# Kernel tuning notes

Hardware: AMD Instinct MI355X
Metric: run time of the kernel (lower is better)

Reference implementation:

```python
import jax, jax.numpy as jnp
import numpy as np

D_MODEL = 1024
N_HEADS = 16
D_HEAD = D_MODEL // N_HEADS
MODES = 32


def setup_inputs() -> dict:
    key = jax.random.key(0)
    ks = jax.random.split(key, 7)
    B, L = 4, 4096
    s = 1.0 / np.sqrt(D_MODEL)
    return {
        "q_in": jax.random.normal(ks[0], (B, L, D_MODEL), dtype=jnp.float32),
        "Wv": jax.random.uniform(ks[1], (D_MODEL, D_MODEL), jnp.float32, -s, s),
        "bv": jax.random.uniform(ks[2], (D_MODEL,), jnp.float32, -s, s),
        "Wo": jax.random.uniform(ks[3], (D_MODEL, D_MODEL), jnp.float32, -s, s),
        "bo": jax.random.uniform(ks[4], (D_MODEL,), jnp.float32, -s, s),
        "w_real": jax.random.normal(ks[5], (N_HEADS, MODES, D_HEAD), dtype=jnp.float32) * 0.02,
        "w_imag": jax.random.normal(ks[6], (N_HEADS, MODES, D_HEAD), dtype=jnp.float32) * 0.02,
    }


def reference(q_in, Wv, bv, Wo, bo, w_real, w_imag):
    B, L, dm = q_in.shape
    # v projection -> [B, H, L, Dh]
    v = (q_in @ Wv.T + bv).reshape(B, L, N_HEADS, D_HEAD).transpose(0, 2, 1, 3)
    # rFFT over time axis; keep only lowest MODES frequencies
    v_ft = jnp.fft.rfft(v, axis=2)                      # [B, H, L//2+1, Dh] complex
    w = (w_real + 1j * w_imag)[None]                    # [1, H, MODES, Dh]
    out_ft = v_ft[:, :, :MODES, :] * w                  # truncated spectrum
    # irfft zero-pads the truncated spectrum up to n//2+1 (== torch's zeros_like + slice-assign)
    out = jnp.fft.irfft(out_ft, n=L, axis=2)            # [B, H, L, Dh]
    out = out.transpose(0, 2, 1, 3).reshape(B, L, dm)
    return out @ Wo.T + bo
```

## Files before the change

### kernel.cpp

```cpp
#include <hip/hip_runtime.h>
#include <math.h>


typedef __attribute__((ext_vector_type(8))) short bf16x8;
typedef __attribute__((ext_vector_type(8))) unsigned short ushort8;
typedef __attribute__((ext_vector_type(4))) float f32x4;

__device__ __forceinline__ unsigned short f2bf(float x) {
    union { float f; unsigned int u; } c; c.f = x;
    unsigned int u = c.u + 0x7FFFu + ((c.u >> 16) & 1u);
    return (unsigned short)(u >> 16);
}

__global__ __launch_bounds__(256) void k_init(unsigned short* __restrict__ F,
                                              unsigned short* __restrict__ G) {
    int idx = blockIdx.x * 256 + threadIdx.x;
    const float w0 = 1.5339807878856412e-3f;
    {
        int j = idx >> 12, t = idx & 4095, k = j >> 1;
        int r = (k * t) & 4095;
        float s, c; sincosf((float)r * w0, &s, &c);
        F[idx] = f2bf((j & 1) ? -s : c);
    }
    {
        int j = idx & 63, k = j >> 1;
        int t = idx >> 6;
        int r = (k * t) & 4095;
        float s, c; sincosf((float)r * w0, &s, &c);
        float ck = (k == 0) ? (1.0f / 4096.0f) : (2.0f / 4096.0f);
        float v = (j & 1) ? ((k == 0) ? 0.0f : -ck * s) : ck * c;
        G[idx] = f2bf(v);
    }
}

__global__ __launch_bounds__(64) void k_dft_fwd(const float* __restrict__ q,
                                                const unsigned short* __restrict__ F,
                                                float* __restrict__ P0) {
    __shared__ __align__(16) unsigned short Ft[64 * 40];
    __shared__ __align__(16) unsigned short qT[32 * 40];
    int blk = blockIdx.x;
    int kp = blk & 15, nt = (blk >> 4) & 31, b = blk >> 9;
    int n0 = nt * 32, t0 = kp * 256;
    int lane = threadIdx.x;
    int lm = lane & 15, q4 = lane >> 4;
    int nn4 = (lane & 7) * 4, th = lane >> 3;
    f32x4 acc[4][2] = {};
    for (int ks = 0; ks < 8; ++ks) {
        int tb = t0 + ks * 32;
        #pragma unroll
        for (int i = 0; i < 4; ++i) {
            ushort8 v = *(const ushort8*)&F[lane * 4096 + tb + i * 8];
            *(ushort8*)&Ft[lane * 40 + i * 8] = v;
        }
        #pragma unroll
        for (int r2 = 0; r2 < 2; ++r2) {
            int p = r2 * 8 + th;
            const float* row0 = &q[(size_t)(b * 4096 + tb + 2 * p) * 1024 + n0 + nn4];
            float4 v0 = *(const float4*)row0;
            float4 v1 = *(const float4*)(row0 + 1024);
            #pragma unroll
            for (int i = 0; i < 4; ++i) {
                float a = (&v0.x)[i], c = (&v1.x)[i];
                unsigned int u = (unsigned int)f2bf(a) | ((unsigned int)f2bf(c) << 16);
                *(unsigned int*)&qT[(nn4 + i) * 40 + 2 * p] = u;
            }
        }
        __syncthreads();
        bf16x8 af[4], bq[2];
        #pragma unroll
        for (int mt = 0; mt < 4; ++mt)
            af[mt] = *(const bf16x8*)&Ft[(mt * 16 + lm) * 40 + q4 * 8];
        #pragma unroll
        for (int ntt = 0; ntt < 2; ++ntt)
            bq[ntt] = *(const bf16x8*)&qT[(ntt * 16 + lm) * 40 + q4 * 8];
        #pragma unroll
        for (int mt = 0; mt < 4; ++mt)
            #pragma unroll
            for (int ntt = 0; ntt < 2; ++ntt)
                acc[mt][ntt] = __builtin_amdgcn_mfma_f32_16x16x32_bf16(
                    af[mt], bq[ntt], acc[mt][ntt], 0, 0, 0);
        __syncthreads();
    }
    size_t base = (size_t)kp * 262144 + (size_t)b * 65536;
    #pragma unroll
    for (int mt = 0; mt < 4; ++mt)
        #pragma unroll
        for (int ntt = 0; ntt < 2; ++ntt)
            #pragma unroll
            for (int r = 0; r < 4; ++r) {
                int j = mt * 16 + q4 * 4 + r;
                int n = n0 + ntt * 16 + lm;
                P0[base + j * 1024 + n] = acc[mt][ntt][r];
            }
}

__global__ __launch_bounds__(256) void k_red16(const float* __restrict__ P0,
                                               unsigned short* __restrict__ Abf) {
    int idx = (blockIdx.x * 256 + threadIdx.x) * 4;
    float4 s = make_float4(0.f, 0.f, 0.f, 0.f);
    #pragma unroll
    for (int p = 0; p < 16; ++p) {
        float4 v = *(const float4*)&P0[(size_t)p * 262144 + idx];
        s.x += v.x; s.y += v.y; s.z += v.z; s.w += v.w;
    }
    ushort4 o;
    o.x = f2bf(s.x); o.y = f2bf(s.y); o.z = f2bf(s.z); o.w = f2bf(s.w);
    *(ushort4*)&Abf[idx] = o;
}

__global__ __launch_bounds__(256) void k_gemm_bt(const unsigned short* __restrict__ Ain,
                                                 const float* __restrict__ Bmat,
                                                 float* __restrict__ P) {
    __shared__ __align__(16) unsigned short At[64 * 40];
    __shared__ __align__(16) unsigned short Wt[128 * 40];
    int blk = blockIdx.x;
    int kp = blk & 7, nt = (blk >> 3) & 7, mt = blk >> 6;
    int m0 = mt * 64, n0 = nt * 128, k0 = kp * 128;
    int tid = threadIdx.x, lane = tid & 63, w = tid >> 6;
    int lm = lane & 15, q4 = lane >> 4;
    int ma = tid >> 2, ka = (tid & 3) * 8;
    int nw = tid >> 1, kw = (tid & 1) * 16;
    f32x4 acc[4][2] = {};
    for (int ks = 0; ks < 4; ++ks) {
        int kb = k0 + ks * 32;
        {
            ushort8 v = *(const ushort8*)&Ain[(m0 + ma) * 1024 + kb + ka];
            *(ushort8*)&At[ma * 40 + ka] = v;
        }
        {
            const float4* wp = (const float4*)&Bmat[(n0 + nw) * 1024 + kb + kw];
            float4 x0 = wp[0], x1 = wp[1], x2 = wp[2], x3 = wp[3];
            ushort8 v0, v1;
            v0[0]=f2bf(x0.x); v0[1]=f2bf(x0.y); v0[2]=f2bf(x0.z); v0[3]=f2bf(x0.w);
            v0[4]=f2bf(x1.x); v0[5]=f2bf(x1.y); v0[6]=f2bf(x1.z); v0[7]=f2bf(x1.w);
            v1[0]=f2bf(x2.x); v1[1]=f2bf(x2.y); v1[2]=f2bf(x2.z); v1[3]=f2bf(x2.w);
            v1[4]=f2bf(x3.x); v1[5]=f2bf(x3.y); v1[6]=f2bf(x3.z); v1[7]=f2bf(x3.w);
            *(ushort8*)&Wt[nw * 40 + kw]     = v0;
            *(ushort8*)&Wt[nw * 40 + kw + 8] = v1;
        }
        __syncthreads();
        bf16x8 af[4], bf[2];
        #pragma unroll
        for (int mti = 0; mti < 4; ++mti)
            af[mti] = *(const bf16x8*)&At[(mti * 16 + lm) * 40 + q4 * 8];
        #pragma unroll
        for (int ntt = 0; ntt < 2; ++ntt)
            bf[ntt] = *(const bf16x8*)&Wt[(w * 32 + ntt * 16 + lm) * 40 + q4 * 8];
        #pragma unroll
        for (int mti = 0; mti < 4; ++mti)
            #pragma unroll
            for (int ntt = 0; ntt < 2; ++ntt)
                acc[mti][ntt] = __builtin_amdgcn_mfma_f32_16x16x32_bf16(
                    af[mti], bf[ntt], acc[mti][ntt], 0, 0, 0);
        __syncthreads();
    }
    #pragma unroll
    for (int mti = 0; mti < 4; ++mti)
        #pragma unroll
        for (int ntt = 0; ntt < 2; ++ntt)
            #pragma unroll
            for (int r = 0; r < 4; ++r) {
                int m = m0 + mti * 16 + q4 * 4 + r;
                int n = n0 + w * 32 + ntt * 16 + lm;
                P[(size_t)kp * 262144 + m * 1024 + n] = acc[mti][ntt][r];
            }
}

__global__ __launch_bounds__(256) void k_cmul(const float* __restrict__ P,
                                              const float* __restrict__ bv,
                                              const float* __restrict__ wr,
                                              const float* __restrict__ wi,
                                              unsigned short* __restrict__ Y) {
    int idx = blockIdx.x * 256 + threadIdx.x;
    int n = idx & 1023, k = (idx >> 10) & 31, b = idx >> 15;
    int rowr = (b * 64 + 2 * k) * 1024 + n;
    int rowi = rowr + 1024;
    float re = 0.f, im = 0.f;
    #pragma unroll
    for (int p = 0; p < 8; ++p) {
        re += P[(size_t)p * 262144 + rowr];
        im += P[(size_t)p * 262144 + rowi];
    }
    if (k == 0) re += 4096.0f * bv[n];
    int h = n >> 6, dh = n & 63;
    float a = wr[(h * 32 + k) * 64 + dh];
    float c = wi[(h * 32 + k) * 64 + dh];
    Y[rowr] = f2bf(re * a - im * c);
    Y[rowi] = f2bf(re * c + im * a);
}

__global__ __launch_bounds__(256) void k_reduce8(const float* __restrict__ P,
                                                 unsigned short* __restrict__ Z) {
    int idx = (blockIdx.x * 256 + threadIdx.x) * 4;
    float4 s = make_float4(0.f, 0.f, 0.f, 0.f);
    #pragma unroll
    for (int p = 0; p < 8; ++p) {
        float4 v = *(const float4*)&P[(size_t)p * 262144 + idx];
        s.x += v.x; s.y += v.y; s.z += v.z; s.w += v.w;
    }
    ushort4 o;
    o.x = f2bf(s.x); o.y = f2bf(s.y); o.z = f2bf(s.z); o.w = f2bf(s.w);
    *(ushort4*)&Z[idx] = o;
}

__global__ __launch_bounds__(256) void k_dft_inv(const unsigned short* __restrict__ G,
                                                 const unsigned short* __restrict__ Zb,
                                                 const float* __restrict__ bo,
                                                 float* __restrict__ out) {
    __shared__ __align__(16) unsigned short Gt[128 * 72];
    __shared__ __align__(16) unsigned short ZT[128 * 72];
    int blk = blockIdx.x;
    int nt = blk & 7, tt = (blk >> 3) & 31, b = blk >> 8;
    int n0 = nt * 128, t0 = tt * 128;
    int tid = threadIdx.x, lane = tid & 63, w = tid >> 6;
    int lm = lane & 15, q4 = lane >> 4;
    {
        int ttl = tid >> 1, jj = (tid & 1) * 32;
        #pragma unroll
        for (int i = 0; i < 4; ++i) {
            ushort8 v = *(const ushort8*)&G[(t0 + ttl) * 64 + jj + i * 8];
            *(ushort8*)&Gt[ttl * 72 + jj + i * 8] = v;
        }
    }
    {
        int jp = tid & 31, hi = tid >> 5;
        int j = jp * 2, nn0 = hi * 16;
        const unsigned short* r0 = &Zb[(b * 64 + j) * 1024 + n0 + nn0];
        const unsigned short* r1 = &Zb[(b * 64 + j + 1) * 1024 + n0 + nn0];
        ushort8 a0 = *(const ushort8*)r0, a1 = *(const ushort8*)(r0 + 8);
        ushort8 b0 = *(const ushort8*)r1, b1 = *(const ushort8*)(r1 + 8);
        #pragma unroll
        for (int i = 0; i < 8; ++i) {
            unsigned int v = (unsigned int)a0[i] | ((unsigned int)b0[i] << 16);
            *(unsigned int*)&ZT[(nn0 + i) * 72 + j] = v;
        }
        #pragma unroll
        for (int i = 0; i < 8; ++i) {
            unsigned int v = (unsigned int)a1[i] | ((unsigned int)b1[i] << 16);
            *(unsigned int*)&ZT[(nn0 + 8 + i) * 72 + j] = v;
        }
    }
    __syncthreads();
    int wt0 = (w >> 1) * 64, wn0 = (w & 1) * 64;
    f32x4 acc[4][4] = {};
    #pragma unroll
    for (int ks = 0; ks < 2; ++ks) {
        bf16x8 af[4], bf[4];
        #pragma unroll
        for (int mt = 0; mt < 4; ++mt)
            af[mt] = *(const bf16x8*)&Gt[(wt0 + mt * 16 + lm) * 72 + ks * 32 + q4 * 8];
        #pragma unroll
        for (int ntt = 0; ntt < 4; ++ntt)
            bf[ntt] = *(const bf16x8*)&ZT[(wn0 + ntt * 16 + lm) * 72 + ks * 32 + q4 * 8];
        #pragma unroll
        for (int mt = 0; mt < 4; ++mt)
            #pragma unroll
            for (int ntt = 0; ntt < 4; ++ntt)
                acc[mt][ntt] = __builtin_amdgcn_mfma_f32_16x16x32_bf16(
                    af[mt], bf[ntt], acc[mt][ntt], 0, 0, 0);
    }
    #pragma unroll
    for (int ntt = 0; ntt < 4; ++ntt) {
        int n = n0 + wn0 + ntt * 16 + lm;
        float bov = bo[n];
        #pragma unroll
        for (int mt = 0; mt < 4; ++mt)
            #pragma unroll
            for (int r = 0; r < 4; ++r) {
                int t = t0 + wt0 + mt * 16 + q4 * 4 + r;
                out[(size_t)(b * 4096 + t) * 1024 + n] = acc[mt][ntt][r] + bov;
            }
    }
}

extern "C" void kernel_launch(void* const* d_in, const int* in_sizes, int n_in,
                              void* d_out, int out_size, void* d_ws, size_t ws_size,
                              hipStream_t stream) {
    const float* q  = (const float*)d_in[0];
    const float* Wv = (const float*)d_in[1];
    const float* bv = (const float*)d_in[2];
    const float* Wo = (const float*)d_in[3];
    const float* bo = (const float*)d_in[4];
    const float* wr = (const float*)d_in[5];
    const float* wi = (const float*)d_in[6];
    float* out = (float*)d_out;

    char* ws = (char*)d_ws;
    unsigned short* F   = (unsigned short*)(ws);
    unsigned short* G   = (unsigned short*)(ws + (512 << 10));
    unsigned short* Abf = (unsigned short*)(ws + (1 << 20));
    unsigned short* Y   = (unsigned short*)(ws + (1 << 20) + (512 << 10));
    unsigned short* Zb  = (unsigned short*)(ws + (2 << 20));
    float*          P0  = (float*)(ws + (3u << 20));
    float*          P1  = (float*)(ws + (19u << 20));
    float*          P2  = (float*)(ws + (27u << 20));

    hipLaunchKernelGGL(k_init,    dim3(1024), dim3(256), 0, stream, F, G);
    hipLaunchKernelGGL(k_dft_fwd, dim3(2048), dim3(64),  0, stream, q, F, P0);
    hipLaunchKernelGGL(k_red16,   dim3(256),  dim3(256), 0, stream, P0, Abf);
    hipLaunchKernelGGL(k_gemm_bt, dim3(256),  dim3(256), 0, stream, Abf, Wv, P1);
    hipLaunchKernelGGL(k_cmul,    dim3(512),  dim3(256), 0, stream, P1, bv, wr, wi, Y);
    hipLaunchKernelGGL(k_gemm_bt, dim3(256),  dim3(256), 0, stream, Y, Wo, P2);
    hipLaunchKernelGGL(k_reduce8, dim3(1024), dim3(256), 0, stream, P2, Zb);
    hipLaunchKernelGGL(k_dft_inv, dim3(1024), dim3(256), 0, stream, G, Zb, bo, out);
}
```

Baseline: 173.5 us.

## Replace split-K GEMMs with full-K direct GEMMs fusing cmul and reduction

```diff
diff --git a/kernel.cpp b/kernel.cpp
--- a/kernel.cpp
+++ b/kernel.cpp
@@ -12,25 +12,33 @@
     return (unsigned short)(u >> 16);
 }
 
-__global__ __launch_bounds__(256) void k_init(unsigned short* __restrict__ F,
-                                              unsigned short* __restrict__ G) {
+__global__ __launch_bounds__(256) void k_init(const float* __restrict__ Wv,
+                                              const float* __restrict__ Wo,
+                                              unsigned short* __restrict__ F,
+                                              unsigned short* __restrict__ G,
+                                              unsigned short* __restrict__ Wvb,
+                                              unsigned short* __restrict__ Wob) {
     int idx = blockIdx.x * 256 + threadIdx.x;
     const float w0 = 1.5339807878856412e-3f;
-    {
-        int j = idx >> 12, t = idx & 4095, k = j >> 1;
-        int r = (k * t) & 4095;
-        float s, c; sincosf((float)r * w0, &s, &c);
-        F[idx] = f2bf((j & 1) ? -s : c);
-    }
-    {
-        int j = idx & 63, k = j >> 1;
-        int t = idx >> 6;
-        int r = (k * t) & 4095;
-        float s, c; sincosf((float)r * w0, &s, &c);
-        float ck = (k == 0) ? (1.0f / 4096.0f) : (2.0f / 4096.0f);
-        float v = (j & 1) ? ((k == 0) ? 0.0f : -ck * s) : ck * c;
-        G[idx] = f2bf(v);
-    }
+    if (idx < 262144) {
+        {
+            int j = idx >> 12, t = idx & 4095, k = j >> 1;
+            int r = (k * t) & 4095;
+            float s, c; sincosf((float)r * w0, &s, &c);
+            F[idx] = f2bf((j & 1) ? -s : c);
+        }
+        {
+            int j = idx & 63, k = j >> 1;
+            int t = idx >> 6;
+            int r = (k * t) & 4095;
+            float s, c; sincosf((float)r * w0, &s, &c);
+            float ck = (k == 0) ? (1.0f / 4096.0f) : (2.0f / 4096.0f);
+            float v = (j & 1) ? ((k == 0) ? 0.0f : -ck * s) : ck * c;
+            G[idx] = f2bf(v);
+        }
+    }
+    if (idx < 1048576) Wvb[idx] = f2bf(Wv[idx]);
+    else               Wob[idx - 1048576] = f2bf(Wo[idx - 1048576]);
 }
 
 __global__ __launch_bounds__(64) void k_dft_fwd(const float* __restrict__ q,
@@ -108,99 +116,54 @@
     *(ushort4*)&Abf[idx] = o;
 }
 
-__global__ __launch_bounds__(256) void k_gemm_bt(const unsigned short* __restrict__ Ain,
-                                                 const float* __restrict__ Bmat,
-                                                 float* __restrict__ P) {
-    __shared__ __align__(16) unsigned short At[64 * 40];
-    __shared__ __align__(16) unsigned short Wt[128 * 40];
+template<int CMUL>
+__global__ __launch_bounds__(256) void k_gemm_small(const unsigned short* __restrict__ Ain,
+                                                    const unsigned short* __restrict__ Wb,
+                                                    const float* __restrict__ bv,
+                                                    const float* __restrict__ wr,
+                                                    const float* __restrict__ wi,
+                                                    unsigned short* __restrict__ Out) {
     int blk = blockIdx.x;
-    int kp = blk & 7, nt = (blk >> 3) & 7, mt = blk >> 6;
-    int m0 = mt * 64, n0 = nt * 128, k0 = kp * 128;
+    int b = blk >> 4, nt = blk & 15;
     int tid = threadIdx.x, lane = tid & 63, w = tid >> 6;
     int lm = lane & 15, q4 = lane >> 4;
-    int ma = tid >> 2, ka = (tid & 3) * 8;
-    int nw = tid >> 1, kw = (tid & 1) * 16;
-    f32x4 acc[4][2] = {};
-    for (int ks = 0; ks < 4; ++ks) {
-        int kb = k0 + ks * 32;
-        {
-            ushort8 v = *(const ushort8*)&Ain[(m0 + ma) * 1024 + kb + ka];
-            *(ushort8*)&At[ma * 40 + ka] = v;
-        }
-        {
-            const float4* wp = (const float4*)&Bmat[(n0 + nw) * 1024 + kb + kw];
-            float4 x0 = wp[0], x1 = wp[1], x2 = wp[2], x3 = wp[3];
-            ushort8 v0, v1;
-            v0[0]=f2bf(x0.x); v0[1]=f2bf(x0.y); v0[2]=f2bf(x0.z); v0[3]=f2bf(x0.w);
-            v0[4]=f2bf(x1.x); v0[5]=f2bf(x1.y); v0[6]=f2bf(x1.z); v0[7]=f2bf(x1.w);
-            v1[0]=f2bf(x2.x); v1[1]=f2bf(x2.y); v1[2]=f2bf(x2.z); v1[3]=f2bf(x2.w);
-            v1[4]=f2bf(x3.x); v1[5]=f2bf(x3.y); v1[6]=f2bf(x3.z); v1[7]=f2bf(x3.w);
-            *(ushort8*)&Wt[nw * 40 + kw]     = v0;
-            *(ushort8*)&Wt[nw * 40 + kw + 8] = v1;
-        }
-        __syncthreads();
-        bf16x8 af[4], bf[2];
-        #pragma unroll
-        for (int mti = 0; mti < 4; ++mti)
-            af[mti] = *(const bf16x8*)&At[(mti * 16 + lm) * 40 + q4 * 8];
-        #pragma unroll
-        for (int ntt = 0; ntt < 2; ++ntt)
-            bf[ntt] = *(const bf16x8*)&Wt[(w * 32 + ntt * 16 + lm) * 40 + q4 * 8];
-        #pragma unroll
-        for (int mti = 0; mti < 4; ++mti)
-            #pragma unroll
-            for (int ntt = 0; ntt < 2; ++ntt)
-                acc[mti][ntt] = __builtin_amdgcn_mfma_f32_16x16x32_bf16(
-                    af[mti], bf[ntt], acc[mti][ntt], 0, 0, 0);
-        __syncthreads();
-    }
-    #pragma unroll
-    for (int mti = 0; mti < 4; ++mti)
-        #pragma unroll
-        for (int ntt = 0; ntt < 2; ++ntt)
-            #pragma unroll
-            for (int r = 0; r < 4; ++r) {
-                int m = m0 + mti * 16 + q4 * 4 + r;
-                int n = n0 + w * 32 + ntt * 16 + lm;
-                P[(size_t)kp * 262144 + m * 1024 + n] = acc[mti][ntt][r];
-            }
-}
-
-__global__ __launch_bounds__(256) void k_cmul(const float* __restrict__ P,
-                                              const float* __restrict__ bv,
-                                              const float* __restrict__ wr,
-                                              const float* __restrict__ wi,
-                                              unsigned short* __restrict__ Y) {
-    int idx = blockIdx.x * 256 + threadIdx.x;
-    int n = idx & 1023, k = (idx >> 10) & 31, b = idx >> 15;
-    int rowr = (b * 64 + 2 * k) * 1024 + n;
-    int rowi = rowr + 1024;
-    float re = 0.f, im = 0.f;
-    #pragma unroll
-    for (int p = 0; p < 8; ++p) {
-        re += P[(size_t)p * 262144 + rowr];
-        im += P[(size_t)p * 262144 + rowi];
-    }
-    if (k == 0) re += 4096.0f * bv[n];
-    int h = n >> 6, dh = n & 63;
-    float a = wr[(h * 32 + k) * 64 + dh];
-    float c = wi[(h * 32 + k) * 64 + dh];
-    Y[rowr] = f2bf(re * a - im * c);
-    Y[rowi] = f2bf(re * c + im * a);
-}
-
-__global__ __launch_bounds__(256) void k_reduce8(const float* __restrict__ P,
-                                                 unsigned short* __restrict__ Z) {
-    int idx = (blockIdx.x * 256 + threadIdx.x) * 4;
-    float4 s = make_float4(0.f, 0.f, 0.f, 0.f);
-    #pragma unroll
-    for (int p = 0; p < 8; ++p) {
-        float4 v = *(const float4*)&P[(size_t)p * 262144 + idx];
-        s.x += v.x; s.y += v.y; s.z += v.z; s.w += v.w;
-    }
-    ushort4 o;
-    o.x = f2bf(s.x); o.y = f2bf(s.y); o.z = f2bf(s.z); o.w = f2bf(s.w);
-    *(ushort4*)&Z[idx] = o;
+    int gn = nt * 64 + w * 16 + lm;
+    const unsigned short* arow = &Ain[(size_t)(b * 64) * 1024 + q4 * 8];
+    const unsigned short* brow = &Wb[(size_t)gn * 1024 + q4 * 8];
+    f32x4 acc[4] = {};
+    #pragma unroll 2
+    for (int it = 0; it < 32; ++it) {
+        int kb = it * 32;
+        bf16x8 bfr = *(const bf16x8*)&brow[kb];
+        #pragma unroll
+        for (int mt4 = 0; mt4 < 4; ++mt4) {
+            bf16x8 afr = *(const bf16x8*)&arow[(mt4 * 16 + lm) * 1024 + kb];
+            acc[mt4] = __builtin_amdgcn_mfma_f32_16x16x32_bf16(afr, bfr, acc[mt4], 0, 0, 0);
+        }
+    }
+    if (CMUL) {
+        int h = gn >> 6, dh = gn & 63;
+        #pragma unroll
+        for (int mt4 = 0; mt4 < 4; ++mt4) {
+            int m0 = mt4 * 16 + q4 * 4;
+            #pragma unroll
+            for (int pp = 0; pp < 2; ++pp) {
+                int m = m0 + 2 * pp, k = m >> 1;
+                float re = acc[mt4][2 * pp], im = acc[mt4][2 * pp + 1];
+                if (m == 0) re += 4096.0f * bv[gn];
+                float a = wr[(h * 32 + k) * 64 + dh];
+                float c = wi[(h * 32 + k) * 64 + dh];
+                Out[(size_t)(b * 64 + m) * 1024 + gn]     = f2bf(re * a - im * c);
+                Out[(size_t)(b * 64 + m + 1) * 1024 + gn] = f2bf(re * c + im * a);
+            }
+        }
+    } else {
+        #pragma unroll
+        for (int mt4 = 0; mt4 < 4; ++mt4)
+            #pragma unroll
+            for (int r = 0; r < 4; ++r)
+                Out[(size_t)(b * 64 + mt4 * 16 + q4 * 4 + r) * 1024 + gn] = f2bf(acc[mt4][r]);
+    }
 }
 
 __global__ __launch_bounds__(256) void k_dft_inv(const unsigned short* __restrict__ G,
@@ -291,16 +254,14 @@
     unsigned short* Abf = (unsigned short*)(ws + (1 << 20));
     unsigned short* Y   = (unsigned short*)(ws + (1 << 20) + (512 << 10));
     unsigned short* Zb  = (unsigned short*)(ws + (2 << 20));
-    float*          P0  = (float*)(ws + (3u << 20));
-    float*          P1  = (float*)(ws + (19u << 20));
-    float*          P2  = (float*)(ws + (27u << 20));
-
-    hipLaunchKernelGGL(k_init,    dim3(1024), dim3(256), 0, stream, F, G);
+    unsigned short* Wvb = (unsigned short*)(ws + (3u << 20));
+    unsigned short* Wob = (unsigned short*)(ws + (5u << 20));
+    float*          P0  = (float*)(ws + (8u << 20));
+
+    hipLaunchKernelGGL(k_init,    dim3(8192), dim3(256), 0, stream, Wv, Wo, F, G, Wvb, Wob);
     hipLaunchKernelGGL(k_dft_fwd, dim3(2048), dim3(64),  0, stream, q, F, P0);
     hipLaunchKernelGGL(k_red16,   dim3(256),  dim3(256), 0, stream, P0, Abf);
-    hipLaunchKernelGGL(k_gemm_bt, dim3(256),  dim3(256), 0, stream, Abf, Wv, P1);
-    hipLaunchKernelGGL(k_cmul,    dim3(512),  dim3(256), 0, stream, P1, bv, wr, wi, Y);
-    hipLaunchKernelGGL(k_gemm_bt, dim3(256),  dim3(256), 0, stream, Y, Wo, P2);
-    hipLaunchKernelGGL(k_reduce8, dim3(1024), dim3(256), 0, stream, P2, Zb);
+    hipLaunchKernelGGL((k_gemm_small<1>), dim3(64), dim3(256), 0, stream, Abf, Wvb, bv, wr, wi, Y);
+    hipLaunchKernelGGL((k_gemm_small<0>), dim3(64), dim3(256), 0, stream, Y, Wob, bv, wr, wi, Zb);
     hipLaunchKernelGGL(k_dft_inv, dim3(1024), dim3(256), 0, stream, G, Zb, bo, out);
 }
```

Measured after the change: 192.6 us. 11.0% more time.

## Replace split-K partial buffers with atomic accumulation and fuse reductions into GEMMs

Applied to the files above, without the earlier changes.

```diff
diff --git a/kernel.cpp b/kernel.cpp
--- a/kernel.cpp
+++ b/kernel.cpp
@@ -12,30 +12,42 @@
     return (unsigned short)(u >> 16);
 }
 
-__global__ __launch_bounds__(256) void k_init(unsigned short* __restrict__ F,
-                                              unsigned short* __restrict__ G) {
+__global__ __launch_bounds__(256) void k_init(const float* __restrict__ Wv,
+                                              const float* __restrict__ Wo,
+                                              unsigned short* __restrict__ F,
+                                              unsigned short* __restrict__ G,
+                                              unsigned short* __restrict__ Wvb,
+                                              unsigned short* __restrict__ Wob,
+                                              float* __restrict__ Af,
+                                              float* __restrict__ Cf,
+                                              float* __restrict__ Zf) {
     int idx = blockIdx.x * 256 + threadIdx.x;
     const float w0 = 1.5339807878856412e-3f;
-    {
-        int j = idx >> 12, t = idx & 4095, k = j >> 1;
-        int r = (k * t) & 4095;
-        float s, c; sincosf((float)r * w0, &s, &c);
-        F[idx] = f2bf((j & 1) ? -s : c);
-    }
-    {
-        int j = idx & 63, k = j >> 1;
-        int t = idx >> 6;
-        int r = (k * t) & 4095;
-        float s, c; sincosf((float)r * w0, &s, &c);
-        float ck = (k == 0) ? (1.0f / 4096.0f) : (2.0f / 4096.0f);
-        float v = (j & 1) ? ((k == 0) ? 0.0f : -ck * s) : ck * c;
-        G[idx] = f2bf(v);
-    }
+    if (idx < 262144) {
+        {
+            int j = idx >> 12, t = idx & 4095, k = j >> 1;
+            int r = (k * t) & 4095;
+            float s, c; sincosf((float)r * w0, &s, &c);
+            F[idx] = f2bf((j & 1) ? -s : c);
+        }
+        {
+            int j = idx & 63, k = j >> 1;
+            int t = idx >> 6;
+            int r = (k * t) & 4095;
+            float s, c; sincosf((float)r * w0, &s, &c);
+            float ck = (k == 0) ? (1.0f / 4096.0f) : (2.0f / 4096.0f);
+            float v = (j & 1) ? ((k == 0) ? 0.0f : -ck * s) : ck * c;
+            G[idx] = f2bf(v);
+        }
+        Af[idx] = 0.0f; Cf[idx] = 0.0f; Zf[idx] = 0.0f;
+    }
+    if (idx < 1048576) Wvb[idx] = f2bf(Wv[idx]);
+    else               Wob[idx - 1048576] = f2bf(Wo[idx - 1048576]);
 }
 
 __global__ __launch_bounds__(64) void k_dft_fwd(const float* __restrict__ q,
                                                 const unsigned short* __restrict__ F,
-                                                float* __restrict__ P0) {
+                                                float* __restrict__ Af) {
     __shared__ __align__(16) unsigned short Ft[64 * 40];
     __shared__ __align__(16) unsigned short qT[32 * 40];
     int blk = blockIdx.x;
@@ -81,7 +93,6 @@
                     af[mt], bq[ntt], acc[mt][ntt], 0, 0, 0);
         __syncthreads();
     }
-    size_t base = (size_t)kp * 262144 + (size_t)b * 65536;
     #pragma unroll
     for (int mt = 0; mt < 4; ++mt)
         #pragma unroll
@@ -90,27 +101,17 @@
             for (int r = 0; r < 4; ++r) {
                 int j = mt * 16 + q4 * 4 + r;
                 int n = n0 + ntt * 16 + lm;
-                P0[base + j * 1024 + n] = acc[mt][ntt][r];
-            }
-}
-
-__global__ __launch_bounds__(256) void k_red16(const float* __restrict__ P0,
-                                               unsigned short* __restrict__ Abf) {
-    int idx = (blockIdx.x * 256 + threadIdx.x) * 4;
-    float4 s = make_float4(0.f, 0.f, 0.f, 0.f);
-    #pragma unroll
-    for (int p = 0; p < 16; ++p) {
-        float4 v = *(const float4*)&P0[(size_t)p * 262144 + idx];
-        s.x += v.x; s.y += v.y; s.z += v.z; s.w += v.w;
-    }
-    ushort4 o;
-    o.x = f2bf(s.x); o.y = f2bf(s.y); o.z = f2bf(s.z); o.w = f2bf(s.w);
-    *(ushort4*)&Abf[idx] = o;
-}
-
-__global__ __launch_bounds__(256) void k_gemm_bt(const unsigned short* __restrict__ Ain,
-                                                 const float* __restrict__ Bmat,
-                                                 float* __restrict__ P) {
+                atomicAdd(&Af[(b * 64 + j) * 1024 + n], acc[mt][ntt][r]);
+            }
+}
+
+template<int FUSE>
+__global__ __launch_bounds__(256) void k_gemm_at(const float* __restrict__ Ain,
+                                                 const unsigned short* __restrict__ Wb,
+                                                 const float* __restrict__ bv,
+                                                 const float* __restrict__ wr,
+                                                 const float* __restrict__ wi,
+                                                 float* __restrict__ Pout) {
     __shared__ __align__(16) unsigned short At[64 * 40];
     __shared__ __align__(16) unsigned short Wt[128 * 40];
     int blk = blockIdx.x;
@@ -123,18 +124,51 @@
     f32x4 acc[4][2] = {};
     for (int ks = 0; ks < 4; ++ks) {
         int kb = k0 + ks * 32;
+        if (!FUSE) {
+            const float* ap = &Ain[(size_t)(m0 + ma) * 1024 + kb + ka];
+            float4 x0 = ((const float4*)ap)[0], x1 = ((const float4*)ap)[1];
+            ushort8 v;
+            v[0]=f2bf(x0.x); v[1]=f2bf(x0.y); v[2]=f2bf(x0.z); v[3]=f2bf(x0.w);
+            v[4]=f2bf(x1.x); v[5]=f2bf(x1.y); v[6]=f2bf(x1.z); v[7]=f2bf(x1.w);
+            *(ushort8*)&At[ma * 40 + ka] = v;
+        } else {
+            int j = ma, je = j & ~1, kmode = je >> 1;
+            int col = kb + ka, h = col >> 6, dh = col & 63;
+            const float* re_p = &Ain[(size_t)(m0 + je) * 1024 + col];
+            float4 e0 = ((const float4*)re_p)[0], e1 = ((const float4*)re_p)[1];
+            float4 o0 = ((const float4*)(re_p + 1024))[0], o1 = ((const float4*)(re_p + 1024))[1];
+            const float* wrp = &wr[(h * 32 + kmode) * 64 + dh];
+            const float* wip = &wi[(h * 32 + kmode) * 64 + dh];
+            float4 a0 = ((const float4*)wrp)[0], a1 = ((const float4*)wrp)[1];
+            float4 c0 = ((const float4*)wip)[0], c1 = ((const float4*)wip)[1];
+            float ev[8], ov[8], av[8], cv[8];
+            #pragma unroll
+            for (int i = 0; i < 4; ++i) {
+                ev[i] = (&e0.x)[i]; ev[4+i] = (&e1.x)[i];
+                ov[i] = (&o0.x)[i]; ov[4+i] = (&o1.x)[i];
+                av[i] = (&a0.x)[i]; av[4+i] = (&a1.x)[i];
+                cv[i] = (&c0.x)[i]; cv[4+i] = (&c1.x)[i];
+            }
+            if (kmode == 0) {
+                float4 b0 = ((const float4*)&bv[col])[0], b1 = ((const float4*)&bv[col])[1];
+                #pragma unroll
+                for (int i = 0; i < 4; ++i) {
+                    ev[i]   += 4096.0f * (&b0.x)[i];
+                    ev[4+i] += 4096.0f * (&b1.x)[i];
+                }
+            }
+            ushort8 v;
+            #pragma unroll
+            for (int i = 0; i < 8; ++i) {
+                float y = (j & 1) ? (ev[i] * cv[i] + ov[i] * av[i])
+                                  : (ev[i] * av[i] - ov[i] * cv[i]);
+                v[i] = f2bf(y);
+            }
+            *(ushort8*)&At[ma * 40 + ka] = v;
+        }
         {
-            ushort8 v = *(const ushort8*)&Ain[(m0 + ma) * 1024 + kb + ka];
-            *(ushort8*)&At[ma * 40 + ka] = v;
-        }
-        {
-            const float4* wp = (const float4*)&Bmat[(n0 + nw) * 1024 + kb + kw];
-            float4 x0 = wp[0], x1 = wp[1], x2 = wp[2], x3 = wp[3];
-            ushort8 v0, v1;
-            v0[0]=f2bf(x0.x); v0[1]=f2bf(x0.y); v0[2]=f2bf(x0.z); v0[3]=f2bf(x0.w);
-            v0[4]=f2bf(x1.x); v0[5]=f2bf(x1.y); v0[6]=f2bf(x1.z); v0[7]=f2bf(x1.w);
-            v1[0]=f2bf(x2.x); v1[1]=f2bf(x2.y); v1[2]=f2bf(x2.z); v1[3]=f2bf(x2.w);
-            v1[4]=f2bf(x3.x); v1[5]=f2bf(x3.y); v1[6]=f2bf(x3.z); v1[7]=f2bf(x3.w);
+            const unsigned short* wp = &Wb[(size_t)(n0 + nw) * 1024 + kb + kw];
+            ushort8 v0 = ((const ushort8*)wp)[0], v1 = ((const ushort8*)wp)[1];
             *(ushort8*)&Wt[nw * 40 + kw]     = v0;
             *(ushort8*)&Wt[nw * 40 + kw + 8] = v1;
         }
@@ -162,49 +196,12 @@
             for (int r = 0; r < 4; ++r) {
                 int m = m0 + mti * 16 + q4 * 4 + r;
                 int n = n0 + w * 32 + ntt * 16 + lm;
-                P[(size_t)kp * 262144 + m * 1024 + n] = acc[mti][ntt][r];
-            }
-}
-
-__global__ __launch_bounds__(256) void k_cmul(const float* __restrict__ P,
-                                              const float* __restrict__ bv,
-                                              const float* __restrict__ wr,
-                                              const float* __restrict__ wi,
-                                              unsigned short* __restrict__ Y) {
-    int idx = blockIdx.x * 256 + threadIdx.x;
-    int n = idx & 1023, k = (idx >> 10) & 31, b = idx >> 15;
-    int rowr = (b * 64 + 2 * k) * 1024 + n;
-    int rowi = rowr + 1024;
-    float re = 0.f, im = 0.f;
-    #pragma unroll
-    for (int p = 0; p < 8; ++p) {
-        re += P[(size_t)p * 262144 + rowr];
-        im += P[(size_t)p * 262144 + rowi];
-    }
-    if (k == 0) re += 4096.0f * bv[n];
-    int h = n >> 6, dh = n & 63;
-    float a = wr[(h * 32 + k) * 64 + dh];
-    float c = wi[(h * 32 + k) * 64 + dh];
-    Y[rowr] = f2bf(re * a - im * c);
-    Y[rowi] = f2bf(re * c + im * a);
-}
-
-__global__ __launch_bounds__(256) void k_reduce8(const float* __restrict__ P,
-                                                 unsigned short* __restrict__ Z) {
-    int idx = (blockIdx.x * 256 + threadIdx.x) * 4;
-    float4 s = make_float4(0.f, 0.f, 0.f, 0.f);
-    #pragma unroll
-    for (int p = 0; p < 8; ++p) {
-        float4 v = *(const float4*)&P[(size_t)p * 262144 + idx];
-        s.x += v.x; s.y += v.y; s.z += v.z; s.w += v.w;
-    }
-    ushort4 o;
-    o.x = f2bf(s.x); o.y = f2bf(s.y); o.z = f2bf(s.z); o.w = f2bf(s.w);
-    *(ushort4*)&Z[idx] = o;
+                atomicAdd(&Pout[(size_t)m * 1024 + n], acc[mti][ntt][r]);
+            }
 }
 
 __global__ __launch_bounds__(256) void k_dft_inv(const unsigned short* __restrict__ G,
-                                                 const unsigned short* __restrict__ Zb,
+                                                 const float* __restrict__ Zf,
                                                  const float* __restrict__ bo,
                                                  float* __restrict__ out) {
     __shared__ __align__(16) unsigned short Gt[128 * 72];
@@ -225,19 +222,19 @@
     {
         int jp = tid & 31, hi = tid >> 5;
         int j = jp * 2, nn0 = hi * 16;
-        const unsigned short* r0 = &Zb[(b * 64 + j) * 1024 + n0 + nn0];
-        const unsigned short* r1 = &Zb[(b * 64 + j + 1) * 1024 + n0 + nn0];
-        ushort8 a0 = *(const ushort8*)r0, a1 = *(const ushort8*)(r0 + 8);
-        ushort8 b0 = *(const ushort8*)r1, b1 = *(const ushort8*)(r1 + 8);
-        #pragma unroll
-        for (int i = 0; i < 8; ++i) {
-            unsigned int v = (unsigned int)a0[i] | ((unsigned int)b0[i] << 16);
+        const float* r0 = &Zf[(size_t)(b * 64 + j) * 1024 + n0 + nn0];
+        const float* r1 = r0 + 1024;
+        float av[16], bvv[16];
+        #pragma unroll
+        for (int i4 = 0; i4 < 4; ++i4) {
+            float4 x = ((const float4*)r0)[i4], y = ((const float4*)r1)[i4];
+            #pragma unroll
+            for (int i = 0; i < 4; ++i) { av[i4*4+i] = (&x.x)[i]; bvv[i4*4+i] = (&y.x)[i]; }
+        }
+        #pragma unroll
+        for (int i = 0; i < 16; ++i) {
+            unsigned int v = (unsigned int)f2bf(av[i]) | ((unsigned int)f2bf(bvv[i]) << 16);
             *(unsigned int*)&ZT[(nn0 + i) * 72 + j] = v;
-        }
-        #pragma unroll
-        for (int i = 0; i < 8; ++i) {
-            unsigned int v = (unsigned int)a1[i] | ((unsigned int)b1[i] << 16);
-            *(unsigned int*)&ZT[(nn0 + 8 + i) * 72 + j] = v;
         }
     }
     __syncthreads();
@@ -288,19 +285,18 @@
     char* ws = (char*)d_ws;
     unsigned short* F   = (unsigned short*)(ws);
     unsigned short* G   = (unsigned short*)(ws + (512 << 10));
-    unsigned short* Abf = (unsigned short*)(ws + (1 << 20));
-    unsigned short* Y   = (unsigned short*)(ws + (1 << 20) + (512 << 10));
-    unsigned short* Zb  = (unsigned short*)(ws + (2 << 20));
-    float*          P0  = (float*)(ws + (3u << 20));
-    float*          P1  = (float*)(ws + (19u << 20));
-    float*          P2  = (float*)(ws + (27u << 20));
-
-    hipLaunchKernelGGL(k_init,    dim3(1024), dim3(256), 0, stream, F, G);
-    hipLaunchKernelGGL(k_dft_fwd, dim3(2048), dim3(64),  0, stream, q, F, P0);
-    hipLaunchKernelGGL(k_red16,   dim3(256),  dim3(256), 0, stream, P0, Abf);
-    hipLaunchKernelGGL(k_gemm_bt, dim3(256),  dim3(256), 0, stream, Abf, Wv, P1);
-    hipLaunchKernelGGL(k_cmul,    dim3(512),  dim3(256), 0, stream, P1, bv, wr, wi, Y);
-    hipLaunchKernelGGL(k_gemm_bt, dim3(256),  dim3(256), 0, stream, Y, Wo, P2);
-    hipLaunchKernelGGL(k_reduce8, dim3(1024), dim3(256), 0, stream, P2, Zb);
-    hipLaunchKernelGGL(k_dft_inv, dim3(1024), dim3(256), 0, stream, G, Zb, bo, out);
-}
+    float*          Af  = (float*)(ws + (1u << 20));
+    float*          Cf  = (float*)(ws + (2u << 20));
+    float*          Zf  = (float*)(ws + (3u << 20));
+    unsigned short* Wvb = (unsigned short*)(ws + (4u << 20));
+    unsigned short* Wob = (unsigned short*)(ws + (6u << 20));
+
+    hipLaunchKernelGGL(k_init,    dim3(8192), dim3(256), 0, stream,
+                       Wv, Wo, F, G, Wvb, Wob, Af, Cf, Zf);
+    hipLaunchKernelGGL(k_dft_fwd, dim3(2048), dim3(64),  0, stream, q, F, Af);
+    hipLaunchKernelGGL((k_gemm_at<0>), dim3(256), dim3(256), 0, stream,
+                       Af, Wvb, bv, wr, wi, Cf);
+    hipLaunchKernelGGL((k_gemm_at<1>), dim3(256), dim3(256), 0, stream,
+                       Cf, Wob, bv, wr, wi, Zf);
+    hipLaunchKernelGGL(k_dft_inv, dim3(1024), dim3(256), 0, stream, G, Zf, bo, out);
+}
```

New measurement: 177.6 us. 1.02x slower.
